# Kernel tuning notes

Hardware: AMD Instinct MI355X
Metric: run time of the kernel (lower is better)

## Reference

```python
import jax, jax.numpy as jnp
import numpy as np

EPS = 1e-6

def setup_inputs() -> dict:
    key = jax.random.key(0)
    ks = jax.random.split(key, 12)
    B, C, H, W = 2, 192, 192, 192
    f = lambda k, s, sc=1.0: jax.random.normal(k, s, dtype=jnp.float32) * sc
    d = {}
    d["x_l"] = f(ks[0], (B, C, H, W))
    d["x_r"] = f(ks[1], (B, C, H, W))
    d["ln_l_w"] = jnp.ones((C,), jnp.float32)
    d["ln_l_b"] = jnp.zeros((C,), jnp.float32)
    d["ln_r_w"] = jnp.ones((C,), jnp.float32)
    d["ln_r_b"] = jnp.zeros((C,), jnp.float32)
    s = C ** -0.5
    d["wq_l"] = f(ks[2], (C, C), s)   # 1x1 conv weights as [out,in]
    d["wq_r"] = f(ks[3], (C, C), s)
    d["wv_l"] = f(ks[4], (C, C), s)
    d["wv_r"] = f(ks[5], (C, C), s)
    d["mlp_w1"] = f(ks[6], (C // 24, C // 3), (C // 3) ** -0.5)
    d["mlp_w2"] = f(ks[7], (C * 2 // 3, C // 24), (C // 24) ** -0.5)
    d["scale_h"] = jnp.ones((1,), jnp.float32)
    d["scale_w"] = jnp.ones((1,), jnp.float32)
    # layer scales are zero-init in the module; use small random so output is nontrivial
    d["ls1"] = f(ks[8], (1, C, 1, 1), 0.1)
    d["ls2"] = f(ks[9], (1, C, 1, 1), 0.1)
    return d

def _ln2d(x, w, b):
    # LayerNorm over channel dim of NCHW
    mu = x.mean(1, keepdims=True)
    var = ((x - mu) ** 2).mean(1, keepdims=True)
    return (x - mu) * jax.lax.rsqrt(var + EPS) * w[None, :, None, None] + b[None, :, None, None]

def _pw(x, w):
    # 1x1 conv, no bias
    return jnp.einsum('bchw,oc->bohw', x, w)

def reference(x_l, x_r, ln_l_w, ln_l_b, ln_r_w, ln_r_b, wq_l, wq_r, wv_l, wv_r,
              mlp_w1, mlp_w2, scale_h, scale_w, ls1, ls2):
    q_l_h, q_l_w, q_l_c = jnp.split(_pw(_ln2d(x_l, ln_l_w, ln_l_b), wq_l), 3, axis=1)
    q_r_h, q_r_w, q_r_c = jnp.split(_pw(_ln2d(x_r, ln_r_w, ln_r_b), wq_r), 3, axis=1)
    v_l_h, v_l_w, v_l_c = jnp.split(_pw(x_l, wv_l), 3, axis=1)
    v_r_h, v_r_w, v_r_c = jnp.split(_pw(x_r, wv_r), 3, axis=1)

    # height axial attention: scores [b, w, h, h']
    attn_h = jnp.einsum('bchw,bcgw->bwhg', q_l_h, q_r_h) * scale_h[0]
    attn_h = jax.nn.softmax(attn_h, axis=-1)
    x_r2l_h = jnp.einsum('bwhg,bcgw->bchw', attn_h, v_r_h)           # [b,c,h,w]
    x_l2r_h = jnp.einsum('bwhg,bchw->bcgw', attn_h, v_l_h)           # attn^T @ v_l

    # width axial attention: scores [b, h, w, w'] (softmax applied separately per direction)
    attn_w = jnp.einsum('bchw,bchv->bhwv', q_l_w, q_r_w) * scale_w[0]
    a1 = jax.nn.softmax(attn_w, axis=-1)
    x_r2l_w = jnp.einsum('bhwv,bchv->bchw', a1, v_r_w)
    a2 = jax.nn.softmax(jnp.swapaxes(attn_w, -1, -2), axis=-1)       # [b,h,v,w]
    x_l2r_w = jnp.einsum('bhvw,bchw->bchv', a2, v_l_w)

    # channel SE branch: sum of the two channel queries, GAP, bottleneck MLP
    p = (q_l_c + q_r_c).mean(axis=(2, 3))                            # [b, c]
    h1 = jax.nn.relu(p @ mlp_w1.T)                                   # [b, c//8]
    a = jax.nn.softmax(h1 @ mlp_w2.T, axis=1)                        # softmax over 2c channels jointly
    attn_l_c, attn_r_c = jnp.split(a, 2, axis=1)
    x_r2l_c = attn_l_c[:, :, None, None] * v_l_c
    x_l2r_c = attn_r_c[:, :, None, None] * v_r_c

    x_r2l = jnp.concatenate([x_r2l_h, x_r2l_w, x_r2l_c], axis=1)
    x_l2r = jnp.concatenate([x_l2r_h, x_l2r_w, x_l2r_c], axis=1)
    out_l = x_r2l * ls1 + x_l
    out_r = x_l2r * ls2 + x_r
    return (out_l, out_r)
```

## Files before the change

kernel.cpp:

```cpp
#include <hip/hip_runtime.h>
#include <stdint.h>

#define NN 36864
#define PL 7077888
#define PL64 2359296
#define TOT 14155776

typedef unsigned short ushort_t;
typedef __attribute__((ext_vector_type(8))) __bf16 bf16x8;
typedef __attribute__((ext_vector_type(4))) float f32x4;
typedef __attribute__((ext_vector_type(4))) unsigned int u32x4;
typedef __attribute__((ext_vector_type(2))) unsigned int u32x2;

__device__ __forceinline__ ushort_t f2bf(float f) {
  unsigned int u = __builtin_bit_cast(unsigned int, f);
  u = (u + 0x7FFFu + ((u >> 16) & 1u)) >> 16;
  return (ushort_t)u;
}
__device__ __forceinline__ float bf2f(ushort_t h) {
  unsigned int u = ((unsigned int)h) << 16;
  return __builtin_bit_cast(float, u);
}
__device__ __forceinline__ bf16x8 lds8(const ushort_t* p) {
  return __builtin_bit_cast(bf16x8, *(const u32x4*)p);
}
__device__ __forceinline__ f32x4 mfma16(bf16x8 a, bf16x8 b, f32x4 c) {
  return __builtin_amdgcn_mfma_f32_16x16x32_bf16(a, b, c, 0, 0, 0);
}
__device__ __forceinline__ unsigned cvtpk(float lo, float hi) {
  unsigned r;
  asm("v_cvt_pk_bf16_f32 %0, %1, %2" : "=v"(r) : "v"(lo), "v"(hi));
  return r;
}

__global__ void k_prep(const float* __restrict__ wq, const float* __restrict__ wv,
                       const float* __restrict__ lnw, const float* __restrict__ lnb,
                       ushort_t* __restrict__ W, float* __restrict__ ab) {
  __shared__ float sa[3], sb[3];
  int r = blockIdx.x, t = threadIdx.x;
  if (r < 192) {
    float w  = wq[r*192 + t];
    float lw = lnw[t], lb = lnb[t];
    W[r*192 + t] = f2bf(w * lw);
    float av = w * lb, bv = -w * lw;
    #pragma unroll
    for (int off = 1; off < 64; off <<= 1) {
      av += __shfl_xor(av, off);
      bv += __shfl_xor(bv, off);
    }
    if ((t & 63) == 0) { sa[t >> 6] = av; sb[t >> 6] = bv; }
    __syncthreads();
    if (t == 0) { ab[r] = sa[0]+sa[1]+sa[2]; ab[192 + r] = sb[0]+sb[1]+sb[2]; }
  } else {
    W[r*192 + t] = f2bf(wv[(r-192)*192 + t]);
  }
}

__global__ __launch_bounds__(512, 2) void k_proj(
    const float* __restrict__ xl, const float* __restrict__ xr,
    const ushort_t* __restrict__ Wl, const ushort_t* __restrict__ Wr,
    const float* __restrict__ abl, const float* __restrict__ abr,
    ushort_t* __restrict__ qhTl, ushort_t* __restrict__ qhTr,
    ushort_t* __restrict__ qwTl, ushort_t* __restrict__ qwTr,
    ushort_t* __restrict__ Vl, ushort_t* __restrict__ Vr,
    float* __restrict__ gpart) {
  __shared__ union {
    ushort_t B[2][6144];
    ushort_t T[13824];
    ushort_t Tv[12800];
  } sm;
  __shared__ float spart[4][192], spart2[4][192];
  __shared__ float smu[192], srs[192];
  __shared__ float gsum[64];

  const int side = blockIdx.y;
  const float*    x  = side ? xr  : xl;
  const ushort_t* W  = side ? Wr  : Wl;
  const float*    ab = side ? abr : abl;
  ushort_t* qhT = side ? qhTr : qhTl;
  ushort_t* qwT = side ? qwTr : qwTl;
  ushort_t* V   = side ? Vr   : Vl;

  const int bh = blockIdx.x;
  const int b  = bh / 192, h = bh % 192;
  const int tid = threadIdx.x;
  const int wave = tid >> 6, lane = tid & 63, lr = lane & 15, lg = lane >> 4;
  const int wm = wave >> 2, wn = wave & 3;

  const int kg0 = tid / 192, n_0 = tid - kg0 * 192;
  const int id1 = 512 + (tid & 255);
  const int kg1 = id1 / 192, n_1 = id1 - kg1 * 192;
  const float* xb0 = x + (size_t)b*PL + (size_t)(kg0*8)*NN + h*192 + n_0;
  const float* xb1 = x + (size_t)b*PL + (size_t)(kg1*8)*NN + h*192 + n_1;
  const int bw0 = n_0*32 + 8*(kg0 ^ ((n_0 >> 1) & 3));
  const int bw1 = n_1*32 + 8*(kg1 ^ ((n_1 >> 1) & 3));
  const int slotR = 8 * (lg ^ ((lr >> 1) & 3));
  const ushort_t* wbase = W + ((size_t)(wm*192 + lr))*192 + lg*8;

  if (tid < 64) gsum[tid] = 0.f;

  const f32x4 fz = {0.f, 0.f, 0.f, 0.f};
  f32x4 acc[12][3];
  #pragma unroll
  for (int mf = 0; mf < 12; ++mf)
    #pragma unroll
    for (int nf = 0; nf < 3; ++nf) acc[mf][nf] = fz;

  float sA0 = 0.f, sB0 = 0.f, sA1 = 0.f, sB1 = 0.f;

  {
    float g0[8], g1[8];
    #pragma unroll
    for (int j = 0; j < 8; ++j) g0[j] = xb0[(size_t)j*NN];
    if (tid < 256) {
      #pragma unroll
      for (int j = 0; j < 8; ++j) g1[j] = xb1[(size_t)j*NN];
    }
    union { ushort_t us[8]; u32x4 v; } t0;
    #pragma unroll
    for (int j = 0; j < 8; ++j) { t0.us[j] = f2bf(g0[j]); sA0 += g0[j]; sB0 += g0[j]*g0[j]; }
    *(u32x4*)&sm.B[0][bw0] = t0.v;
    if (tid < 256) {
      union { ushort_t us[8]; u32x4 v; } t1;
      #pragma unroll
      for (int j = 0; j < 8; ++j) { t1.us[j] = f2bf(g1[j]); sA1 += g1[j]; sB1 += g1[j]*g1[j]; }
      *(u32x4*)&sm.B[0][bw1] = t1.v;
    }
  }
  __syncthreads();

  for (int ks = 0; ks < 6; ++ks) {
    const int cur = ks & 1, nxt = cur ^ 1;
    float g0[8], g1[8];
    if (ks < 5) {
      const int k0n = (ks + 1) * 32;
      #pragma unroll
      for (int j = 0; j < 8; ++j) g0[j] = xb0[(size_t)(k0n + j)*NN];
      if (tid < 256) {
        #pragma unroll
        for (int j = 0; j < 8; ++j) g1[j] = xb1[(size_t)(k0n + j)*NN];
      }
    }
    bf16x8 bfr[3];
    #pragma unroll
    for (int nf = 0; nf < 3; ++nf)
      bfr[nf] = lds8(&sm.B[cur][(wn*48 + nf*16 + lr)*32 + slotR]);
    bf16x8 afr[12];
    #pragma unroll
    for (int mf = 0; mf < 12; ++mf)
      afr[mf] = lds8(wbase + mf*3072 + ks*32);
    #pragma unroll
    for (int mf = 0; mf < 12; ++mf) {
      #pragma unroll
      for (int nf = 0; nf < 3; ++nf) acc[mf][nf] = mfma16(afr[mf], bfr[nf], acc[mf][nf]);
    }
    if (ks < 5) {
      union { ushort_t us[8]; u32x4 v; } t0;
      #pragma unroll
      for (int j = 0; j < 8; ++j) { t0.us[j] = f2bf(g0[j]); sA0 += g0[j]; sB0 += g0[j]*g0[j]; }
      *(u32x4*)&sm.B[nxt][bw0] = t0.v;
      if (tid < 256) {
        union { ushort_t us[8]; u32x4 v; } t1;
        #pragma unroll
        for (int j = 0; j < 8; ++j) { t1.us[j] = f2bf(g1[j]); sA1 += g1[j]; sB1 += g1[j]*g1[j]; }
        *(u32x4*)&sm.B[nxt][bw1] = t1.v;
      }
    }
    __syncthreads();
  }

  spart[kg0][n_0] = sA0; spart2[kg0][n_0] = sB0;
  if (tid < 256) { spart[kg1][n_1] = sA1; spart2[kg1][n_1] = sB1; }
  __syncthreads();
  if (tid < 192) {
    float s  = spart[0][tid] + spart[1][tid] + spart[2][tid] + spart[3][tid];
    float s2 = spart2[0][tid] + spart2[1][tid] + spart2[2][tid] + spart2[3][tid];
    float mu = s * (1.f/192.f);
    float var = s2 * (1.f/192.f) - mu*mu;
    smu[tid] = mu;
    srs[tid] = rsqrtf(var + 1e-6f);
  }
  __syncthreads();

  if (wm == 0) {
    float rst[3], mrs[3];
    #pragma unroll
    for (int nf = 0; nf < 3; ++nf) {
      int n_ = wn*48 + nf*16 + lr;
      float rs = srs[n_];
      rst[nf] = rs;
      mrs[nf] = smu[n_] * rs;
    }
    #pragma unroll
    for (int mf = 0; mf < 12; ++mf) {
      #pragma unroll
      for (int i = 0; i < 4; ++i) {
        int m = mf*16 + lg*4 + i;
        float a_ = ab[m], bb = ab[192 + m];
        #pragma unroll
        for (int nf = 0; nf < 3; ++nf)
          acc[mf][nf][i] = acc[mf][nf][i]*rst[nf] + bb*mrs[nf] + a_;
      }
    }
  }

  if (wm == 0) {
    #pragma unroll
    for (int mf = 0; mf < 4; ++mf)
      #pragma unroll
      for (int nf = 0; nf < 3; ++nf)
        #pragma unroll
        for (int i = 0; i < 4; ++i)
          sm.T[(wn*48 + nf*16 + lr)*72 + mf*16 + lg*4 + i] = f2bf(acc[mf][nf][i]);
  }
  __syncthreads();
  #pragma unroll
  for (int p = 0; p < 3; ++p) {
    int id = p*512 + tid, n = id >> 3, c8 = id & 7;
    u32x4 v = *(const u32x4*)&sm.T[n*72 + c8*8];
    *(u32x4*)&qhT[(((size_t)b*192 + n)*192 + h)*64 + c8*8] = v;
  }
  __syncthreads();

  if (wm == 0) {
    #pragma unroll
    for (int mf = 4; mf < 8; ++mf)
      #pragma unroll
      for (int nf = 0; nf < 3; ++nf)
        #pragma unroll
        for (int i = 0; i < 4; ++i)
          sm.T[(wn*48 + nf*16 + lr)*72 + (mf-4)*16 + lg*4 + i] = f2bf(acc[mf][nf][i]);
  }
  __syncthreads();
  #pragma unroll
  for (int p = 0; p < 3; ++p) {
    int id = p*512 + tid, n = id >> 3, c8 = id & 7;
    u32x4 v = *(const u32x4*)&sm.T[n*72 + c8*8];
    *(u32x4*)&qwT[(((size_t)b*192 + h)*192 + n)*64 + c8*8] = v;
  }

  if (wm == 0) {
    #pragma unroll
    for (int mf = 8; mf < 12; ++mf) {
      #pragma unroll
      for (int i = 0; i < 4; ++i) {
        float part = acc[mf][0][i] + acc[mf][1][i] + acc[mf][2][i];
        #pragma unroll
        for (int off = 1; off < 16; off <<= 1) part += __shfl_xor(part, off);
        if (lr == 0) atomicAdd(&gsum[(mf-8)*16 + lg*4 + i], part);
      }
    }
  }
  __syncthreads();
  if (tid < 64) gpart[(((size_t)side*2 + b)*192 + h)*64 + tid] = gsum[tid];

  #pragma unroll
  for (int ch = 0; ch < 3; ++ch) {
    __syncthreads();
    if (wm == 1) {
      #pragma unroll
      for (int q = 0; q < 4; ++q) {
        int mf = ch*4 + q;
        #pragma unroll
        for (int nf = 0; nf < 3; ++nf)
          #pragma unroll
          for (int i = 0; i < 4; ++i)
            sm.Tv[(q*16 + lg*4 + i)*200 + wn*48 + nf*16 + lr] = f2bf(acc[mf][nf][i]);
      }
    }
    __syncthreads();
    #pragma unroll
    for (int p = 0; p < 3; ++p) {
      int id = p*512 + tid;
      int cc = id / 24, seg = id % 24;
      u32x4 v = *(const u32x4*)&sm.Tv[cc*200 + seg*8];
      *(u32x4*)&V[((size_t)b*192 + ch*64 + cc)*NN + h*192 + seg*8] = v;
    }
  }
}

__global__ void k_repack_v(const ushort_t* __restrict__ Vl, const ushort_t* __restrict__ Vr,
                           ushort_t* __restrict__ vhTl, ushort_t* __restrict__ vhTr) {
  __shared__ ushort_t Ls[64*72];
  const ushort_t* V = blockIdx.y ? Vr : Vl;
  ushort_t* out = blockIdx.y ? vhTr : vhTl;
  int bx = blockIdx.x;
  int b = bx / 576, rem = bx % 576;
  int c = rem / 9, tt = rem % 9;
  int h0 = (tt/3)*64, w0 = (tt%3)*64;
  int tid = threadIdx.x;
  #pragma unroll
  for (int i = 0; i < 2; ++i) {
    int idx = tid + 256*i;
    int hh = idx >> 3, wb = idx & 7;
    *(u32x4*)&Ls[hh*72 + wb*8] =
      *(const u32x4*)&V[(size_t)(b*192 + c)*NN + (h0+hh)*192 + w0 + wb*8];
  }
  __syncthreads();
  #pragma unroll
  for (int i = 0; i < 2; ++i) {
    int idx = tid + 256*i;
    int ww = idx >> 3, hb = idx & 7;
    union { ushort_t us[8]; u32x4 v; } tu;
    #pragma unroll
    for (int j = 0; j < 8; ++j) tu.us[j] = Ls[(hb*8+j)*72 + ww];
    *(u32x4*)&out[(size_t)(b*64 + c)*NN + (w0+ww)*192 + h0 + hb*8] = tu.v;
  }
}

__global__ __launch_bounds__(256, 2) void k_attn(
    const ushort_t* __restrict__ qhTl, const ushort_t* __restrict__ qhTr,
    const ushort_t* __restrict__ qwTl, const ushort_t* __restrict__ qwTr,
    const ushort_t* __restrict__ Vl,  const ushort_t* __restrict__ Vr,
    const ushort_t* __restrict__ vhTl, const ushort_t* __restrict__ vhTr,
    const float* __restrict__ sch, const float* __restrict__ scw,
    ushort_t* __restrict__ Oh1, ushort_t* __restrict__ Oh2,
    ushort_t* __restrict__ Ow1, ushort_t* __restrict__ Ow2) {
  __shared__ ushort_t Qsl[192*64];
  __shared__ ushort_t Qsr[192*64];
  __shared__ ushort_t Vs[64*192];
  __shared__ float md[192*2];

  const int tid = threadIdx.x;
  const int wave = tid >> 6, lane = tid & 63, lr = lane & 15, lg = lane >> 4;
  const int bx = blockIdx.x;
  const int mode = bx / 384;
  const int b = (bx % 384) / 192, s0 = bx % 192;
  const float scl = (mode ? scw : sch)[0];

  const ushort_t* ql = (mode ? qwTl : qhTl) + (size_t)(b*192 + s0)*12288;
  const ushort_t* qr = (mode ? qwTr : qhTr) + (size_t)(b*192 + s0)*12288;
  const ushort_t* vr = mode ? Vr + (size_t)(b*192 + 64)*NN + s0*192
                            : vhTr + (size_t)b*PL64 + s0*192;
  const ushort_t* vl = mode ? Vl + (size_t)(b*192 + 64)*NN + s0*192
                            : vhTl + (size_t)b*PL64 + s0*192;
  ushort_t* og1 = (mode ? Ow1 : Oh1) + (size_t)(b*192 + s0)*12288;
  ushort_t* og2 = (mode ? Ow2 : Oh2) + (size_t)(b*192 + s0)*12288;

  #pragma unroll
  for (int i = 0; i < 6; ++i) {
    int idx = tid + 256*i;
    int r = idx >> 3, sl = idx & 7;
    int dq = r*64 + ((sl ^ (r & 7)) << 3);
    *(u32x4*)&Qsl[dq] = *(const u32x4*)&ql[idx*8];
    *(u32x4*)&Qsr[dq] = *(const u32x4*)&qr[idx*8];
    int c = idx / 24, gs = idx % 24;
    *(u32x4*)&Vs[c*192 + ((gs ^ (c & 7)) << 3)] = *(const u32x4*)&vr[(size_t)c*NN + gs*8];
  }
  __syncthreads();

  const f32x4 fz = {0.f, 0.f, 0.f, 0.f};
  f32x4 acc[12][3];
  unsigned pk[3][12][2];

  auto qk = [&](bool swap) {
    const ushort_t* A  = swap ? Qsl : Qsr;
    const ushort_t* Bq = swap ? Qsr : Qsl;
    #pragma unroll
    for (int mf = 0; mf < 12; ++mf)
      #pragma unroll
      for (int nf = 0; nf < 3; ++nf) acc[mf][nf] = fz;
    __builtin_amdgcn_s_setprio(1);
    #pragma unroll
    for (int kh = 0; kh < 2; ++kh) {
      bf16x8 bq[3];
      #pragma unroll
      for (int nf = 0; nf < 3; ++nf) {
        int r = wave*48 + nf*16 + lr;
        bq[nf] = lds8(&Bq[r*64 + (((kh*4 + lg) ^ (r & 7)) << 3)]);
      }
      #pragma unroll
      for (int mf = 0; mf < 12; ++mf) {
        int r = mf*16 + lr;
        bf16x8 aq = lds8(&A[r*64 + (((kh*4 + lg) ^ (r & 7)) << 3)]);
        #pragma unroll
        for (int nf = 0; nf < 3; ++nf) acc[mf][nf] = mfma16(aq, bq[nf], acc[mf][nf]);
      }
    }
    __builtin_amdgcn_s_setprio(0);
  };

  auto smpack = [&](bool store_md) {
    #pragma unroll
    for (int nf = 0; nf < 3; ++nf) {
      float mx = -3.4e38f;
      #pragma unroll
      for (int mf = 0; mf < 12; ++mf)
        #pragma unroll
        for (int i = 0; i < 4; ++i) {
          float v = acc[mf][nf][i] * scl;
          acc[mf][nf][i] = v;
          mx = fmaxf(mx, v);
        }
      mx = fmaxf(mx, __shfl_xor(mx, 16));
      mx = fmaxf(mx, __shfl_xor(mx, 32));
      float den = 0.f;
      #pragma unroll
      for (int mf = 0; mf < 12; ++mf)
        #pragma unroll
        for (int i = 0; i < 4; ++i) {
          float e = __expf(acc[mf][nf][i] - mx);
          acc[mf][nf][i] = e;
          den += e;
        }
      den += __shfl_xor(den, 16);
      den += __shfl_xor(den, 32);
      float rd = 1.f / den;
      if (store_md && lg == 0) {
        int col = wave*48 + nf*16 + lr;
        md[col*2] = mx; md[col*2+1] = rd;
      }
      #pragma unroll
      for (int mf = 0; mf < 12; ++mf) {
        pk[nf][mf][0] = cvtpk(acc[mf][nf][0]*rd, acc[mf][nf][1]*rd);
        pk[nf][mf][1] = cvtpk(acc[mf][nf][2]*rd, acc[mf][nf][3]*rd);
      }
    }
  };

  auto pv = [&](unsigned obf[4][3][2]) {
    f32x4 o[4][3];
    #pragma unroll
    for (int mf = 0; mf < 4; ++mf)
      #pragma unroll
      for (int nf = 0; nf < 3; ++nf) o[mf][nf] = fz;
    const int sA = lr + 32*(lg & 1), sB = sA + 16;
    const bool hi = (lg >> 1) != 0;
    __builtin_amdgcn_s_setprio(1);
    #pragma unroll
    for (int ks = 0; ks < 6; ++ks) {
      bf16x8 av[4];
      #pragma unroll
      for (int mf = 0; mf < 4; ++mf) {
        int c = mf*16 + lr;
        av[mf] = lds8(&Vs[c*192 + (((4*ks + lg) ^ (c & 7)) << 3)]);
      }
      #pragma unroll
      for (int nf = 0; nf < 3; ++nf) {
        unsigned w0a = (unsigned)__shfl((int)pk[nf][2*ks  ][0], sA);
        unsigned w0b = (unsigned)__shfl((int)pk[nf][2*ks+1][0], sA);
        unsigned w1a = (unsigned)__shfl((int)pk[nf][2*ks  ][1], sA);
        unsigned w1b = (unsigned)__shfl((int)pk[nf][2*ks+1][1], sA);
        unsigned w2a = (unsigned)__shfl((int)pk[nf][2*ks  ][0], sB);
        unsigned w2b = (unsigned)__shfl((int)pk[nf][2*ks+1][0], sB);
        unsigned w3a = (unsigned)__shfl((int)pk[nf][2*ks  ][1], sB);
        unsigned w3b = (unsigned)__shfl((int)pk[nf][2*ks+1][1], sB);
        u32x4 wv = { hi ? w0b : w0a, hi ? w1b : w1a, hi ? w2b : w2a, hi ? w3b : w3a };
        bf16x8 bp = __builtin_bit_cast(bf16x8, wv);
        #pragma unroll
        for (int mf = 0; mf < 4; ++mf) o[mf][nf] = mfma16(av[mf], bp, o[mf][nf]);
      }
    }
    __builtin_amdgcn_s_setprio(0);
    #pragma unroll
    for (int mf = 0; mf < 4; ++mf)
      #pragma unroll
      for (int nf = 0; nf < 3; ++nf) {
        obf[mf][nf][0] = cvtpk(o[mf][nf][0], o[mf][nf][1]);
        obf[mf][nf][1] = cvtpk(o[mf][nf][2], o[mf][nf][3]);
      }
  };

  auto owrite = [&](unsigned obf[4][3][2]) {
    char* Ot = (char*)Qsl;
    #pragma unroll
    for (int mf = 0; mf < 4; ++mf)
      #pragma unroll
      for (int nf = 0; nf < 3; ++nf) {
        int col = wave*48 + nf*16 + lr;
        int byte = col*128 + ((mf*32 + lg*8) ^ ((col & 7) << 4));
        u32x2 v = { obf[mf][nf][0], obf[mf][nf][1] };
        *(u32x2*)(Ot + byte) = v;
      }
  };

  auto ostore = [&](ushort_t* og) {
    const char* Ot = (const char*)Qsl;
    #pragma unroll
    for (int it = 0; it < 6; ++it) {
      int id = tid + 256*it;
      int col = id >> 3, s = id & 7;
      int byte = col*128 + ((s*16) ^ ((col & 7) << 4));
      u32x4 v = *(const u32x4*)(Ot + byte);
      *(u32x4*)&og[(size_t)col*64 + s*8] = v;
    }
  };

  qk(false);
  smpack(true);
  unsigned o1bf[4][3][2];
  pv(o1bf);

  u32x4 vlr[6];
  #pragma unroll
  for (int i = 0; i < 6; ++i) {
    int idx = tid + 256*i;
    int c = idx / 24, gs = idx % 24;
    vlr[i] = *(const u32x4*)&vl[(size_t)c*NN + gs*8];
  }

  qk(true);
  __syncthreads();

  owrite(o1bf);
  #pragma unroll
  for (int i = 0; i < 6; ++i) {
    int idx = tid + 256*i;
    int c = idx / 24, gs = idx % 24;
    *(u32x4*)&Vs[c*192 + ((gs ^ (c & 7)) << 3)] = vlr[i];
  }

  if (mode == 0) {
    #pragma unroll
    for (int mf = 0; mf < 12; ++mf)
      #pragma unroll
      for (int i = 0; i < 4; ++i) {
        int row = mf*16 + lg*4 + i;
        float m_ = md[row*2], rd_ = md[row*2+1];
        #pragma unroll
        for (int nf = 0; nf < 3; ++nf)
          acc[mf][nf][i] = __expf(acc[mf][nf][i]*scl - m_) * rd_;
      }
    #pragma unroll
    for (int nf = 0; nf < 3; ++nf)
      #pragma unroll
      for (int mf = 0; mf < 12; ++mf) {
        pk[nf][mf][0] = cvtpk(acc[mf][nf][0], acc[mf][nf][1]);
        pk[nf][mf][1] = cvtpk(acc[mf][nf][2], acc[mf][nf][3]);
      }
  } else {
    smpack(false);
  }
  __syncthreads();

  ostore(og1);
  unsigned o2bf[4][3][2];
  pv(o2bf);
  __syncthreads();
  owrite(o2bf);
  __syncthreads();
  ostore(og2);
}

__global__ void k_se(const float* __restrict__ gpart, const float* __restrict__ w1,
                     const float* __restrict__ w2, float* __restrict__ sea) {
  __shared__ float p[2][64];
  __shared__ float h1[2][8];
  __shared__ float lgt[2][128];
  __shared__ float mred[2], dred[2];
  int t = threadIdx.x;
  if (t < 128) {
    int b = t >> 6, c = t & 63;
    float s = 0.f;
    for (int side = 0; side < 2; ++side)
      for (int h = 0; h < 192; ++h)
        s += gpart[(((size_t)side*2 + b)*192 + h)*64 + c];
    p[b][c] = s * (1.f/36864.f);
  }
  __syncthreads();
  if (t < 16) {
    int bb = t >> 3, j = t & 7;
    float s = 0.f;
    for (int k = 0; k < 64; ++k) s += p[bb][k] * w1[j*64 + k];
    h1[bb][j] = fmaxf(s, 0.f);
  }
  __syncthreads();
  {
    int bb = t >> 7, o = t & 127;
    float s = 0.f;
    #pragma unroll
    for (int j = 0; j < 8; ++j) s += h1[bb][j] * w2[o*8 + j];
    lgt[bb][o] = s;
  }
  __syncthreads();
  if (t < 2) {
    float mx = -3.4e38f;
    for (int o = 0; o < 128; ++o) mx = fmaxf(mx, lgt[t][o]);
    float d = 0.f;
    for (int o = 0; o < 128; ++o) d += __expf(lgt[t][o] - mx);
    mred[t] = mx; dred[t] = d;
  }
  __syncthreads();
  {
    int bb = t >> 7, o = t & 127;
    sea[bb*128 + o] = __expf(lgt[bb][o] - mred[bb]) / dred[bb];
  }
}

__global__ __launch_bounds__(256, 4) void k_ep(
    const ushort_t* __restrict__ Oh1, const ushort_t* __restrict__ Oh2,
    const ushort_t* __restrict__ Ow1, const ushort_t* __restrict__ Ow2,
    const ushort_t* __restrict__ Vl, const ushort_t* __restrict__ Vr,
    const float* __restrict__ sea,
    const float* __restrict__ xl, const float* __restrict__ xr,
    const float* __restrict__ ls1, const float* __restrict__ ls2,
    float* __restrict__ out) {
  __shared__ ushort_t T[192*64];
  const int gid = blockIdx.x;
  const int h = gid % 192;
  const int b = (gid / 192) % 2;
  const int dir = gid / 384;
  const int tid = threadIdx.x;
  const float* xin = dir ? xr : xl;
  const float* ls  = dir ? ls2 : ls1;
  const ushort_t* Oh = dir ? Oh2 : Oh1;
  const ushort_t* Ow = dir ? Ow2 : Ow1;
  const ushort_t* Vv = dir ? Vr  : Vl;
  float* outp = out + (size_t)dir*TOT;

  const int c0 = (tid / 24) * 8, wseg = tid % 24, w0 = wseg * 8;
  const int Srd = (wseg & 7) << 4;

  auto flush = [&](int cbase) {
    if (tid < 192) {
      u32x4 r[8];
      #pragma unroll
      for (int j = 0; j < 8; ++j)
        r[j] = *(const u32x4*)((const char*)T + (w0 + j)*128 + ((c0*2) ^ Srd));
      #pragma unroll
      for (int k = 0; k < 8; ++k) {
        int c = cbase + c0 + k;
        float lsv = ls[c];
        size_t oo = (size_t)(b*192 + c)*NN + h*192 + w0;
        f32x4 xa = *(const f32x4*)&xin[oo];
        f32x4 xb2 = *(const f32x4*)&xin[oo + 4];
        f32x4 r0, r1;
        #pragma unroll
        for (int j = 0; j < 4; ++j) r0[j] = bf2f(((const ushort_t*)&r[j])[k])*lsv + xa[j];
        #pragma unroll
        for (int j = 0; j < 4; ++j) r1[j] = bf2f(((const ushort_t*)&r[4+j])[k])*lsv + xb2[j];
        *(f32x4*)&outp[oo] = r0;
        *(f32x4*)&outp[oo + 4] = r1;
      }
    }
  };

  {
    const ushort_t* ohb = Oh + ((size_t)b*192*192 + h)*64;
    #pragma unroll
    for (int it = 0; it < 6; ++it) {
      int id = tid + 256*it;
      int w = id >> 3, s = id & 7;
      u32x4 v = *(const u32x4*)&ohb[(size_t)w*12288 + s*8];
      *(u32x4*)((char*)T + w*128 + ((s*16) ^ (((w >> 3) & 7) << 4))) = v;
    }
  }
  __syncthreads();
  flush(0);
  __syncthreads();

  {
    const ushort_t* owb = Ow + ((size_t)b*192 + h)*12288;
    #pragma unroll
    for (int it = 0; it < 6; ++it) {
      int id = tid + 256*it;
      int w = id >> 3, s = id & 7;
      u32x4 v = *(const u32x4*)&owb[id*8];
      *(u32x4*)((char*)T + w*128 + ((s*16) ^ (((w >> 3) & 7) << 4))) = v;
    }
  }
  __syncthreads();
  flush(64);

  #pragma unroll
  for (int it = 0; it < 6; ++it) {
    int id = tid + 256*it;
    int cc = id / 24, ws = (id % 24) * 8;
    float lsv = ls[128 + cc] * sea[b*128 + dir*64 + cc];
    size_t oo = (size_t)(b*192 + 128 + cc)*NN + h*192 + ws;
    u32x4 sv = *(const u32x4*)&Vv[(size_t)(b*192 + 128 + cc)*NN + h*192 + ws];
    const ushort_t* sp = (const ushort_t*)&sv;
    f32x4 xa = *(const f32x4*)&xin[oo];
    f32x4 xb2 = *(const f32x4*)&xin[oo + 4];
    f32x4 r0, r1;
    #pragma unroll
    for (int j = 0; j < 4; ++j) r0[j] = bf2f(sp[j])*lsv + xa[j];
    #pragma unroll
    for (int j = 0; j < 4; ++j) r1[j] = bf2f(sp[4+j])*lsv + xb2[j];
    *(f32x4*)&outp[oo] = r0;
    *(f32x4*)&outp[oo + 4] = r1;
  }
}

extern "C" void kernel_launch(void* const* d_in, const int* in_sizes, int n_in,
                              void* d_out, int out_size, void* d_ws, size_t ws_size,
                              hipStream_t stream) {
  const float* x_l  = (const float*)d_in[0];
  const float* x_r  = (const float*)d_in[1];
  const float* lnlw = (const float*)d_in[2];
  const float* lnlb = (const float*)d_in[3];
  const float* lnrw = (const float*)d_in[4];
  const float* lnrb = (const float*)d_in[5];
  const float* wq_l = (const float*)d_in[6];
  const float* wq_r = (const float*)d_in[7];
  const float* wv_l = (const float*)d_in[8];
  const float* wv_r = (const float*)d_in[9];
  const float* w1   = (const float*)d_in[10];
  const float* w2   = (const float*)d_in[11];
  const float* sch  = (const float*)d_in[12];
  const float* scw  = (const float*)d_in[13];
  const float* ls1  = (const float*)d_in[14];
  const float* ls2  = (const float*)d_in[15];
  float* out = (float*)d_out;

  char* ws = (char*)d_ws;
  size_t off = 0;
  auto alloc = [&](size_t bytes) {
    char* p = ws + off;
    off += (bytes + 255) & ~(size_t)255;
    return p;
  };
  ushort_t* Vl   = (ushort_t*)alloc((size_t)2*192*NN*2);
  ushort_t* Vr   = (ushort_t*)alloc((size_t)2*192*NN*2);
  ushort_t* qhTl = (ushort_t*)alloc((size_t)2*64*NN*2);
  ushort_t* qhTr = (ushort_t*)alloc((size_t)2*64*NN*2);
  ushort_t* qwTl = (ushort_t*)alloc((size_t)2*64*NN*2);
  ushort_t* qwTr = (ushort_t*)alloc((size_t)2*64*NN*2);
  ushort_t* vhTl = (ushort_t*)alloc((size_t)2*64*NN*2);
  ushort_t* vhTr = (ushort_t*)alloc((size_t)2*64*NN*2);
  ushort_t* Oh1  = (ushort_t*)alloc((size_t)2*64*NN*2);
  ushort_t* Oh2  = (ushort_t*)alloc((size_t)2*64*NN*2);
  ushort_t* Ow1  = (ushort_t*)alloc((size_t)2*64*NN*2);
  ushort_t* Ow2  = (ushort_t*)alloc((size_t)2*64*NN*2);
  ushort_t* Wl   = (ushort_t*)alloc((size_t)384*192*2);
  ushort_t* Wr   = (ushort_t*)alloc((size_t)384*192*2);
  float* abl = (float*)alloc(384*4);
  float* abr = (float*)alloc(384*4);
  float* gpart = (float*)alloc((size_t)2*2*192*64*4);
  float* sea = (float*)alloc(2*128*4);
  (void)in_sizes; (void)n_in; (void)out_size; (void)ws_size;

  k_prep<<<384, 192, 0, stream>>>(wq_l, wv_l, lnlw, lnlb, Wl, abl);
  k_prep<<<384, 192, 0, stream>>>(wq_r, wv_r, lnrw, lnrb, Wr, abr);
  k_proj<<<dim3(384, 2), 512, 0, stream>>>(x_l, x_r, Wl, Wr, abl, abr,
                                           qhTl, qhTr, qwTl, qwTr, Vl, Vr, gpart);
  k_repack_v<<<dim3(1152, 2), 256, 0, stream>>>(Vl, Vr, vhTl, vhTr);
  k_attn<<<768, 256, 0, stream>>>(qhTl, qhTr, qwTl, qwTr, Vl, Vr, vhTl, vhTr,
                                  sch, scw, Oh1, Oh2, Ow1, Ow2);
  k_se<<<1, 256, 0, stream>>>(gpart, w1, w2, sea);
  k_ep<<<768, 256, 0, stream>>>(Oh1, Oh2, Ow1, Ow2, Vl, Vr, sea,
                                x_l, x_r, ls1, ls2, out);
}
```

Baseline: 280.6 us.

## Retile projection kernel to 64-column blocks with full-K staging and higher occupancy

The projection kernel now splits each (batch,row) into three 64-wide column tiles and handles both sides in one flattened grid of 2304 blocks. Each block loads its whole 192-channel x slice into LDS at once instead of double-buffering K-chunks. Each wave computes 48 output rows by 64 columns, which shrinks the accumulator register footprint and allows launch bounds of 4 blocks per CU. The channel-SE partial sums are now per column tile, and k_se is widened to reduce the larger gpart array in parallel. The cost is more blocks and more total loads of the weight matrix.

```diff
diff --git a/kernel.cpp b/kernel.cpp
--- a/kernel.cpp
+++ b/kernel.cpp
@@ -56,7 +56,7 @@
   }
 }
 
-__global__ __launch_bounds__(512, 2) void k_proj(
+__global__ __launch_bounds__(512, 4) void k_proj(
     const float* __restrict__ xl, const float* __restrict__ xr,
     const ushort_t* __restrict__ Wl, const ushort_t* __restrict__ Wr,
     const float* __restrict__ abl, const float* __restrict__ abr,
@@ -65,15 +65,20 @@
     ushort_t* __restrict__ Vl, ushort_t* __restrict__ Vr,
     float* __restrict__ gpart) {
   __shared__ union {
-    ushort_t B[2][6144];
-    ushort_t T[13824];
-    ushort_t Tv[12800];
+    ushort_t B[64*192];
+    ushort_t T[64*72];
   } sm;
-  __shared__ float spart[4][192], spart2[4][192];
-  __shared__ float smu[192], srs[192];
+  __shared__ float spart[8][64], spart2[8][64];
+  __shared__ float smu[64], srs[64];
   __shared__ float gsum[64];
 
-  const int side = blockIdx.y;
+  const int bx = blockIdx.x;
+  const int side = bx & 1;
+  const int r0 = bx >> 1;
+  const int ws = r0 % 3, bh = r0 / 3;
+  const int b = bh / 192, h = bh % 192;
+  const int w0 = ws * 64;
+
   const float*    x  = side ? xr  : xl;
   const ushort_t* W  = side ? Wr  : Wl;
   const float*    ab = side ? abr : abl;
@@ -81,201 +86,183 @@
   ushort_t* qwT = side ? qwTr : qwTl;
   ushort_t* V   = side ? Vr   : Vl;
 
-  const int bh = blockIdx.x;
-  const int b  = bh / 192, h = bh % 192;
   const int tid = threadIdx.x;
   const int wave = tid >> 6, lane = tid & 63, lr = lane & 15, lg = lane >> 4;
-  const int wm = wave >> 2, wn = wave & 3;
-
-  const int kg0 = tid / 192, n_0 = tid - kg0 * 192;
-  const int id1 = 512 + (tid & 255);
-  const int kg1 = id1 / 192, n_1 = id1 - kg1 * 192;
-  const float* xb0 = x + (size_t)b*PL + (size_t)(kg0*8)*NN + h*192 + n_0;
-  const float* xb1 = x + (size_t)b*PL + (size_t)(kg1*8)*NN + h*192 + n_1;
-  const int bw0 = n_0*32 + 8*(kg0 ^ ((n_0 >> 1) & 3));
-  const int bw1 = n_1*32 + 8*(kg1 ^ ((n_1 >> 1) & 3));
-  const int slotR = 8 * (lg ^ ((lr >> 1) & 3));
-  const ushort_t* wbase = W + ((size_t)(wm*192 + lr))*192 + lg*8;
 
   if (tid < 64) gsum[tid] = 0.f;
 
-  const f32x4 fz = {0.f, 0.f, 0.f, 0.f};
-  f32x4 acc[12][3];
-  #pragma unroll
-  for (int mf = 0; mf < 12; ++mf)
-    #pragma unroll
-    for (int nf = 0; nf < 3; ++nf) acc[mf][nf] = fz;
-
-  float sA0 = 0.f, sB0 = 0.f, sA1 = 0.f, sB1 = 0.f;
-
   {
-    float g0[8], g1[8];
-    #pragma unroll
-    for (int j = 0; j < 8; ++j) g0[j] = xb0[(size_t)j*NN];
-    if (tid < 256) {
-      #pragma unroll
-      for (int j = 0; j < 8; ++j) g1[j] = xb1[(size_t)j*NN];
-    }
-    union { ushort_t us[8]; u32x4 v; } t0;
-    #pragma unroll
-    for (int j = 0; j < 8; ++j) { t0.us[j] = f2bf(g0[j]); sA0 += g0[j]; sB0 += g0[j]*g0[j]; }
-    *(u32x4*)&sm.B[0][bw0] = t0.v;
-    if (tid < 256) {
-      union { ushort_t us[8]; u32x4 v; } t1;
-      #pragma unroll
-      for (int j = 0; j < 8; ++j) { t1.us[j] = f2bf(g1[j]); sA1 += g1[j]; sB1 += g1[j]*g1[j]; }
-      *(u32x4*)&sm.B[0][bw1] = t1.v;
-    }
-  }
-  __syncthreads();
-
-  for (int ks = 0; ks < 6; ++ks) {
-    const int cur = ks & 1, nxt = cur ^ 1;
-    float g0[8], g1[8];
-    if (ks < 5) {
-      const int k0n = (ks + 1) * 32;
-      #pragma unroll
-      for (int j = 0; j < 8; ++j) g0[j] = xb0[(size_t)(k0n + j)*NN];
-      if (tid < 256) {
-        #pragma unroll
-        for (int j = 0; j < 8; ++j) g1[j] = xb1[(size_t)(k0n + j)*NN];
-      }
-    }
-    bf16x8 bfr[3];
-    #pragma unroll
-    for (int nf = 0; nf < 3; ++nf)
-      bfr[nf] = lds8(&sm.B[cur][(wn*48 + nf*16 + lr)*32 + slotR]);
-    bf16x8 afr[12];
-    #pragma unroll
-    for (int mf = 0; mf < 12; ++mf)
-      afr[mf] = lds8(wbase + mf*3072 + ks*32);
-    #pragma unroll
-    for (int mf = 0; mf < 12; ++mf) {
-      #pragma unroll
-      for (int nf = 0; nf < 3; ++nf) acc[mf][nf] = mfma16(afr[mf], bfr[nf], acc[mf][nf]);
-    }
-    if (ks < 5) {
-      union { ushort_t us[8]; u32x4 v; } t0;
-      #pragma unroll
-      for (int j = 0; j < 8; ++j) { t0.us[j] = f2bf(g0[j]); sA0 += g0[j]; sB0 += g0[j]*g0[j]; }
-      *(u32x4*)&sm.B[nxt][bw0] = t0.v;
-      if (tid < 256) {
-        union { ushort_t us[8]; u32x4 v; } t1;
-        #pragma unroll
-        for (int j = 0; j < 8; ++j) { t1.us[j] = f2bf(g1[j]); sA1 += g1[j]; sB1 += g1[j]*g1[j]; }
-        *(u32x4*)&sm.B[nxt][bw1] = t1.v;
-      }
-    }
-    __syncthreads();
-  }
-
-  spart[kg0][n_0] = sA0; spart2[kg0][n_0] = sB0;
-  if (tid < 256) { spart[kg1][n_1] = sA1; spart2[kg1][n_1] = sB1; }
-  __syncthreads();
-  if (tid < 192) {
-    float s  = spart[0][tid] + spart[1][tid] + spart[2][tid] + spart[3][tid];
-    float s2 = spart2[0][tid] + spart2[1][tid] + spart2[2][tid] + spart2[3][tid];
+    const int kq = wave, n = lane;
+    const float* xb = x + (size_t)b*PL + h*192 + w0 + n;
+    float gv[24];
+    #pragma unroll
+    for (int s = 0; s < 6; ++s)
+      #pragma unroll
+      for (int j = 0; j < 4; ++j)
+        gv[s*4 + j] = xb[(size_t)(s*32 + kq*4 + j)*NN];
+    float sA = 0.f, sB = 0.f;
+    char* Bb = (char*)sm.B;
+    const int slot = 16*((kq >> 1) ^ ((n >> 1) & 3)) + 8*(kq & 1);
+    #pragma unroll
+    for (int s = 0; s < 6; ++s) {
+      union { ushort_t us[4]; u32x2 v; } t2;
+      #pragma unroll
+      for (int j = 0; j < 4; ++j) {
+        float g = gv[s*4 + j];
+        t2.us[j] = f2bf(g);
+        sA += g; sB += g*g;
+      }
+      *(u32x2*)(Bb + n*384 + s*64 + slot) = t2.v;
+    }
+    spart[kq][n] = sA; spart2[kq][n] = sB;
+  }
+  __syncthreads();
+
+  if (tid < 64) {
+    float s = 0.f, s2 = 0.f;
+    #pragma unroll
+    for (int q = 0; q < 8; ++q) { s += spart[q][tid]; s2 += spart2[q][tid]; }
     float mu = s * (1.f/192.f);
     float var = s2 * (1.f/192.f) - mu*mu;
     smu[tid] = mu;
     srs[tid] = rsqrtf(var + 1e-6f);
   }
-  __syncthreads();
-
-  if (wm == 0) {
-    float rst[3], mrs[3];
-    #pragma unroll
-    for (int nf = 0; nf < 3; ++nf) {
-      int n_ = wn*48 + nf*16 + lr;
+
+  const ushort_t* wbase = W + (size_t)(48*wave + lr)*192 + lg*8;
+  const char* Bb = (const char*)sm.B;
+  const f32x4 fz = {0.f, 0.f, 0.f, 0.f};
+  f32x4 acc[3][4];
+  #pragma unroll
+  for (int mf = 0; mf < 3; ++mf)
+    #pragma unroll
+    for (int nf = 0; nf < 4; ++nf) acc[mf][nf] = fz;
+
+  #pragma unroll
+  for (int ks = 0; ks < 6; ++ks) {
+    bf16x8 bfr[4];
+    #pragma unroll
+    for (int nf = 0; nf < 4; ++nf) {
+      int n_ = nf*16 + lr;
+      bfr[nf] = lds8((const ushort_t*)(Bb + n_*384 + ks*64 + 16*(lg ^ ((n_ >> 1) & 3))));
+    }
+    bf16x8 afr[3];
+    #pragma unroll
+    for (int mf = 0; mf < 3; ++mf)
+      afr[mf] = lds8(wbase + (size_t)mf*16*192 + ks*32);
+    #pragma unroll
+    for (int mf = 0; mf < 3; ++mf)
+      #pragma unroll
+      for (int nf = 0; nf < 4; ++nf)
+        acc[mf][nf] = mfma16(afr[mf], bfr[nf], acc[mf][nf]);
+  }
+  __syncthreads();
+
+  if (wave < 4) {
+    float rst[4], mrs[4];
+    #pragma unroll
+    for (int nf = 0; nf < 4; ++nf) {
+      int n_ = nf*16 + lr;
       float rs = srs[n_];
       rst[nf] = rs;
       mrs[nf] = smu[n_] * rs;
     }
     #pragma unroll
-    for (int mf = 0; mf < 12; ++mf) {
+    for (int mf = 0; mf < 3; ++mf) {
+      int m = 48*wave + 16*mf + 4*lg;
       #pragma unroll
       for (int i = 0; i < 4; ++i) {
-        int m = mf*16 + lg*4 + i;
-        float a_ = ab[m], bb = ab[192 + m];
-        #pragma unroll
-        for (int nf = 0; nf < 3; ++nf)
+        float a_ = ab[m + i], bb = ab[192 + m + i];
+        #pragma unroll
+        for (int nf = 0; nf < 4; ++nf)
           acc[mf][nf][i] = acc[mf][nf][i]*rst[nf] + bb*mrs[nf] + a_;
       }
     }
   }
 
-  if (wm == 0) {
-    #pragma unroll
-    for (int mf = 0; mf < 4; ++mf)
-      #pragma unroll
-      for (int nf = 0; nf < 3; ++nf)
-        #pragma unroll
-        for (int i = 0; i < 4; ++i)
-          sm.T[(wn*48 + nf*16 + lr)*72 + mf*16 + lg*4 + i] = f2bf(acc[mf][nf][i]);
-  }
-  __syncthreads();
-  #pragma unroll
-  for (int p = 0; p < 3; ++p) {
-    int id = p*512 + tid, n = id >> 3, c8 = id & 7;
-    u32x4 v = *(const u32x4*)&sm.T[n*72 + c8*8];
-    *(u32x4*)&qhT[(((size_t)b*192 + n)*192 + h)*64 + c8*8] = v;
-  }
-  __syncthreads();
-
-  if (wm == 0) {
-    #pragma unroll
-    for (int mf = 4; mf < 8; ++mf)
-      #pragma unroll
-      for (int nf = 0; nf < 3; ++nf)
-        #pragma unroll
-        for (int i = 0; i < 4; ++i)
-          sm.T[(wn*48 + nf*16 + lr)*72 + (mf-4)*16 + lg*4 + i] = f2bf(acc[mf][nf][i]);
-  }
-  __syncthreads();
-  #pragma unroll
-  for (int p = 0; p < 3; ++p) {
-    int id = p*512 + tid, n = id >> 3, c8 = id & 7;
-    u32x4 v = *(const u32x4*)&sm.T[n*72 + c8*8];
-    *(u32x4*)&qwT[(((size_t)b*192 + h)*192 + n)*64 + c8*8] = v;
-  }
-
-  if (wm == 0) {
-    #pragma unroll
-    for (int mf = 8; mf < 12; ++mf) {
-      #pragma unroll
-      for (int i = 0; i < 4; ++i) {
-        float part = acc[mf][0][i] + acc[mf][1][i] + acc[mf][2][i];
-        #pragma unroll
-        for (int off = 1; off < 16; off <<= 1) part += __shfl_xor(part, off);
-        if (lr == 0) atomicAdd(&gsum[(mf-8)*16 + lg*4 + i], part);
-      }
-    }
-  }
-  __syncthreads();
-  if (tid < 64) gpart[(((size_t)side*2 + b)*192 + h)*64 + tid] = gsum[tid];
+  char* Tb = (char*)sm.T;
+  if (wave < 4) {
+    #pragma unroll
+    for (int mf = 0; mf < 3; ++mf) {
+      int base = 48*wave + 16*mf;
+      if ((base >> 6) == 0) {
+        #pragma unroll
+        for (int nf = 0; nf < 4; ++nf) {
+          u32x2 v = { cvtpk(acc[mf][nf][0], acc[mf][nf][1]),
+                      cvtpk(acc[mf][nf][2], acc[mf][nf][3]) };
+          *(u32x2*)(Tb + (nf*16 + lr)*144 + (base + 4*lg)*2) = v;
+        }
+      }
+    }
+  }
+  __syncthreads();
+  {
+    int w = tid >> 3, c8 = tid & 7;
+    u32x4 v = *(const u32x4*)(Tb + w*144 + c8*16);
+    *(u32x4*)&qhT[(((size_t)b*192 + w0 + w)*192 + h)*64 + c8*8] = v;
+  }
+  __syncthreads();
+
+  if (wave < 4) {
+    #pragma unroll
+    for (int mf = 0; mf < 3; ++mf) {
+      int base = 48*wave + 16*mf;
+      if ((base >> 6) == 1) {
+        #pragma unroll
+        for (int nf = 0; nf < 4; ++nf) {
+          u32x2 v = { cvtpk(acc[mf][nf][0], acc[mf][nf][1]),
+                      cvtpk(acc[mf][nf][2], acc[mf][nf][3]) };
+          *(u32x2*)(Tb + (nf*16 + lr)*144 + (base - 64 + 4*lg)*2) = v;
+        }
+      }
+    }
+  }
+  __syncthreads();
+  {
+    int w = tid >> 3, c8 = tid & 7;
+    u32x4 v = *(const u32x4*)(Tb + w*144 + c8*16);
+    *(u32x4*)&qwT[(((size_t)b*192 + h)*192 + w0 + w)*64 + c8*8] = v;
+  }
+  __syncthreads();
 
   #pragma unroll
   for (int ch = 0; ch < 3; ++ch) {
+    if (wave >= 4) {
+      #pragma unroll
+      for (int mf = 0; mf < 3; ++mf) {
+        int vc = 48*(wave - 4) + 16*mf;
+        if ((vc >> 6) == ch) {
+          int cc = vc - 64*ch + 4*lg;
+          #pragma unroll
+          for (int nf = 0; nf < 4; ++nf)
+            #pragma unroll
+            for (int i = 0; i < 4; ++i)
+              *(ushort_t*)(Tb + (cc + i)*144 + (nf*16 + lr)*2) = f2bf(acc[mf][nf][i]);
+        }
+      }
+    } else if (ch == 0) {
+      #pragma unroll
+      for (int mf = 0; mf < 3; ++mf) {
+        int base = 48*wave + 16*mf;
+        if ((base >> 6) == 2) {
+          #pragma unroll
+          for (int i = 0; i < 4; ++i) {
+            float part = acc[mf][0][i] + acc[mf][1][i] + acc[mf][2][i] + acc[mf][3][i];
+            #pragma unroll
+            for (int off = 1; off < 16; off <<= 1) part += __shfl_xor(part, off);
+            if (lr == 0) atomicAdd(&gsum[base - 128 + 4*lg + i], part);
+          }
+        }
+      }
+    }
     __syncthreads();
-    if (wm == 1) {
-      #pragma unroll
-      for (int q = 0; q < 4; ++q) {
-        int mf = ch*4 + q;
-        #pragma unroll
-        for (int nf = 0; nf < 3; ++nf)
-          #pragma unroll
-          for (int i = 0; i < 4; ++i)
-            sm.Tv[(q*16 + lg*4 + i)*200 + wn*48 + nf*16 + lr] = f2bf(acc[mf][nf][i]);
-      }
-    }
+    {
+      int cc = tid >> 3, w8 = tid & 7;
+      u32x4 v = *(const u32x4*)(Tb + cc*144 + w8*16);
+      *(u32x4*)&V[((size_t)b*192 + ch*64 + cc)*NN + h*192 + w0 + w8*8] = v;
+    }
+    if (ch == 0 && tid < 64)
+      gpart[(((size_t)(side*2 + b)*192 + h)*3 + ws)*64 + tid] = gsum[tid];
     __syncthreads();
-    #pragma unroll
-    for (int p = 0; p < 3; ++p) {
-      int id = p*512 + tid;
-      int cc = id / 24, seg = id % 24;
-      u32x4 v = *(const u32x4*)&sm.Tv[cc*200 + seg*8];
-      *(u32x4*)&V[((size_t)b*192 + ch*64 + cc)*NN + h*192 + seg*8] = v;
-    }
   }
 }
 
@@ -544,18 +531,23 @@
 
 __global__ void k_se(const float* __restrict__ gpart, const float* __restrict__ w1,
                      const float* __restrict__ w2, float* __restrict__ sea) {
+  __shared__ float psum[256];
   __shared__ float p[2][64];
   __shared__ float h1[2][8];
   __shared__ float lgt[2][128];
   __shared__ float mred[2], dred[2];
   int t = threadIdx.x;
+  {
+    int b = t >> 7, sideh = (t >> 6) & 1, c = t & 63;
+    float s = 0.f;
+    for (int j = 0; j < 576; ++j)
+      s += gpart[((size_t)(sideh*2 + b)*576 + j)*64 + c];
+    psum[t] = s;
+  }
+  __syncthreads();
   if (t < 128) {
     int b = t >> 6, c = t & 63;
-    float s = 0.f;
-    for (int side = 0; side < 2; ++side)
-      for (int h = 0; h < 192; ++h)
-        s += gpart[(((size_t)side*2 + b)*192 + h)*64 + c];
-    p[b][c] = s * (1.f/36864.f);
+    p[b][c] = (psum[b*128 + c] + psum[b*128 + 64 + c]) * (1.f/36864.f);
   }
   __syncthreads();
   if (t < 16) {
@@ -726,14 +718,14 @@
   ushort_t* Wr   = (ushort_t*)alloc((size_t)384*192*2);
   float* abl = (float*)alloc(384*4);
   float* abr = (float*)alloc(384*4);
-  float* gpart = (float*)alloc((size_t)2*2*192*64*4);
+  float* gpart = (float*)alloc((size_t)2*2*576*64*4);
   float* sea = (float*)alloc(2*128*4);
   (void)in_sizes; (void)n_in; (void)out_size; (void)ws_size;
 
   k_prep<<<384, 192, 0, stream>>>(wq_l, wv_l, lnlw, lnlb, Wl, abl);
   k_prep<<<384, 192, 0, stream>>>(wq_r, wv_r, lnrw, lnrb, Wr, abr);
-  k_proj<<<dim3(384, 2), 512, 0, stream>>>(x_l, x_r, Wl, Wr, abl, abr,
-                                           qhTl, qhTr, qwTl, qwTr, Vl, Vr, gpart);
+  k_proj<<<2304, 512, 0, stream>>>(x_l, x_r, Wl, Wr, abl, abr,
+                                   qhTl, qhTr, qwTl, qwTr, Vl, Vr, gpart);
   k_repack_v<<<dim3(1152, 2), 256, 0, stream>>>(Vl, Vr, vhTl, vhTr);
   k_attn<<<768, 256, 0, stream>>>(qhTl, qhTr, qwTl, qwTr, Vl, Vr, vhTl, vhTr,
                                   sch, scw, Oh1, Oh2, Ow1, Ow2);
```

Result: faster. 232.8 us (-17.0%).
